# Performance work log

Hardware: AMD Instinct MI355X
Metric: run time of the kernel (lower is better)

Reference implementation:

```python
import jax, jax.numpy as jnp
import numpy as np

T, D, H = 2048, 2048, 16
C = D // H  # head dim = 128

def setup_inputs() -> dict:
    key = jax.random.key(0)
    k1, k2, k3 = jax.random.split(key, 3)
    x = jax.random.normal(k1, (T, D), dtype=jnp.float32)
    W_attn = jax.random.normal(k2, (3 * D, D), dtype=jnp.float32) * 0.02
    W_proj = jax.random.normal(k3, (D, D), dtype=jnp.float32) * 0.02
    return {"x": x, "W_attn": W_attn, "W_proj": W_proj}

def reference(x, W_attn, W_proj):
    # c_attn: per-token Linear -> [T, 3D]
    qkv = x @ W_attn.T
    q, k, v = jnp.split(qkv, 3, axis=-1)  # each [T, D]
    # [T, D] -> [H, T, C]
    q = q.reshape(T, H, C).transpose(1, 0, 2)
    k = k.reshape(T, H, C).transpose(1, 0, 2)
    v = v.reshape(T, H, C).transpose(1, 0, 2)
    # raw scores [H, T, T]
    scores = jnp.einsum('htc,hsc->hts', q, k)
    causal_mask = jnp.tril(jnp.ones((1, T, T))) == 0
    scores = jnp.where(causal_mask, float('-inf'), scores)
    orig_dtype = scores.dtype
    # NOTE: original scales AFTER masking, inside softmax, in fp32
    attn = jax.nn.softmax(scores.astype(jnp.float32) / jnp.sqrt(jnp.float32(C)), axis=-1)
    attn = attn.astype(orig_dtype)
    out = attn @ v  # [H, T, C]
    out = out.transpose(1, 0, 2).reshape(T, D)
    return out @ W_proj.T
```

## Files before the change

### kernel.cpp

```cpp
#include <hip/hip_runtime.h>
#include <hip/hip_bf16.h>
#include <stdint.h>

typedef __attribute__((ext_vector_type(8))) __bf16 bf16x8;
typedef __attribute__((ext_vector_type(4))) float f32x4;
typedef __attribute__((ext_vector_type(4))) unsigned int u32x4;
typedef __attribute__((ext_vector_type(4))) unsigned short u16x4;

__device__ __forceinline__ unsigned short f2bf(float f) {
  union { float f; unsigned int u; } v; v.f = f;
  unsigned int r = v.u + 0x7fffu + ((v.u >> 16) & 1u);
  return (unsigned short)(r >> 16);
}

__device__ __forceinline__ void gload_lds16(const void* g, void* l) {
  __builtin_amdgcn_global_load_lds(
      (const __attribute__((address_space(1))) unsigned int*)g,
      (__attribute__((address_space(3))) unsigned int*)l, 16, 0, 0);
}

__global__ __launch_bounds__(256) void cast_f32_bf16(const float* __restrict__ in,
                                                     unsigned short* __restrict__ out,
                                                     int n) {
  int i = (blockIdx.x * 256 + threadIdx.x) * 4;
  if (i >= n) return;
  f32x4 v = *(const f32x4*)&in[i];
  u16x4 o;
  o[0] = f2bf(v[0]); o[1] = f2bf(v[1]); o[2] = f2bf(v[2]); o[3] = f2bf(v[3]);
  *(u16x4*)&out[i] = o;
}

template<int OUT_BF16>
__global__ __launch_bounds__(256) void gemm_bt(const unsigned short* __restrict__ A,
                                               const unsigned short* __restrict__ B,
                                               void* __restrict__ Cv,
                                               int M, int N, int K) {
  __shared__ unsigned short As[128 * 32];
  __shared__ unsigned short Bs[128 * 32];

  const int tid  = threadIdx.x;
  const int lane = tid & 63;
  const int wave = tid >> 6;
  const int wr = (wave >> 1) * 64;
  const int wc = (wave & 1) * 64;
  const int row0 = blockIdx.y * 128;
  const int col0 = blockIdx.x * 128;
  const int l16 = lane & 15;
  const int lk  = (lane >> 4) * 8;

  const int srow = lane >> 2;
  const int sc   = (lane & 3) * 8;

  f32x4 acc[4][4] = {};

  for (int k0 = 0; k0 < K; k0 += 32) {
    __syncthreads();
#pragma unroll
    for (int i = 0; i < 2; ++i) {
      int t = wave * 2 + i;
      int r = t * 16 + srow;
      gload_lds16(&A[(size_t)(row0 + r) * K + k0 + sc], &As[t * 512]);
      gload_lds16(&B[(size_t)(col0 + r) * K + k0 + sc], &Bs[t * 512]);
    }
    __syncthreads();

    bf16x8 af[4], bfr[4];
#pragma unroll
    for (int i = 0; i < 4; ++i) af[i]  = *(const bf16x8*)&As[(wr + i * 16 + l16) * 32 + lk];
#pragma unroll
    for (int i = 0; i < 4; ++i) bfr[i] = *(const bf16x8*)&Bs[(wc + i * 16 + l16) * 32 + lk];
#pragma unroll
    for (int i = 0; i < 4; ++i)
#pragma unroll
      for (int j = 0; j < 4; ++j)
        acc[i][j] = __builtin_amdgcn_mfma_f32_16x16x32_bf16(af[i], bfr[j], acc[i][j], 0, 0, 0);
  }

  const int orow = (lane >> 4) * 4;
#pragma unroll
  for (int i = 0; i < 4; ++i)
#pragma unroll
    for (int j = 0; j < 4; ++j)
#pragma unroll
      for (int r = 0; r < 4; ++r) {
        size_t gr = row0 + wr + i * 16 + orow + r;
        size_t gc = col0 + wc + j * 16 + l16;
        float v = acc[i][j][r];
        if (OUT_BF16) ((unsigned short*)Cv)[gr * N + gc] = f2bf(v);
        else          ((float*)Cv)[gr * N + gc] = v;
      }
}

__global__ __launch_bounds__(256, 2) void attn_kernel(const unsigned short* __restrict__ qkv,
                                                      unsigned short* __restrict__ ctx) {
  __shared__ unsigned short Ks[64][136];
  __shared__ unsigned short VTs[128][72];
  __shared__ unsigned short Ps[4][16][72];

  const int tid  = threadIdx.x;
  const int lane = tid & 63;
  const int w    = tid >> 6;
  const int l16  = lane & 15;
  const int lk8  = (lane >> 4) * 8;

  const int flat = blockIdx.x + blockIdx.y * 32;
  int h, qb;
  if (flat < 256) { h = flat >> 5; qb = flat & 31; }
  else            { int f2 = flat - 256; h = 8 + (f2 >> 5); qb = 31 - (f2 & 31); }

  const int qrow = qb * 64 + w * 16;

  bf16x8 qf[4];
#pragma unroll
  for (int kk = 0; kk < 4; ++kk)
    qf[kk] = *(const bf16x8*)&qkv[(size_t)(qrow + l16) * 6144 + h * 128 + kk * 32 + lk8];

  f32x4 o[8] = {};
  float m[4], lsum[4];
#pragma unroll
  for (int r = 0; r < 4; ++r) { m[r] = -1e30f; lsum[r] = 0.f; }

  const float sscale = 0.08838834764831845f * 1.4426950408889634f;
  const int qg0 = qrow + (lane >> 4) * 4;

  const int t0v = (tid & 15) * 4;
  const int c0v = (tid >> 4) * 8;

  const int nkb = qb + 1;
  for (int kb = 0; kb < nkb; ++kb) {
    u32x4 kreg[4], vreg[4];
#pragma unroll
    for (int it = 0; it < 4; ++it) {
      int idx = it * 256 + tid;
      int row = idx >> 4, c0 = (idx & 15) * 8;
      kreg[it] = *(const u32x4*)&qkv[(size_t)(kb * 64 + row) * 6144 + 2048 + h * 128 + c0];
    }
#pragma unroll
    for (int r = 0; r < 4; ++r)
      vreg[r] = *(const u32x4*)&qkv[(size_t)(kb * 64 + t0v + r) * 6144 + 4096 + h * 128 + c0v];

    __syncthreads();

#pragma unroll
    for (int it = 0; it < 4; ++it) {
      int idx = it * 256 + tid;
      int row = idx >> 4, c0 = (idx & 15) * 8;
      *(u32x4*)&Ks[row][c0] = kreg[it];
    }
    {
      const unsigned short* p0 = (const unsigned short*)&vreg[0];
      const unsigned short* p1 = (const unsigned short*)&vreg[1];
      const unsigned short* p2 = (const unsigned short*)&vreg[2];
      const unsigned short* p3 = (const unsigned short*)&vreg[3];
#pragma unroll
      for (int j = 0; j < 8; ++j) {
        u16x4 wv; wv[0] = p0[j]; wv[1] = p1[j]; wv[2] = p2[j]; wv[3] = p3[j];
        *(u16x4*)&VTs[c0v + j][t0v] = wv;
      }
    }
    __syncthreads();

    f32x4 s[4] = {};
#pragma unroll
    for (int kk = 0; kk < 4; ++kk)
#pragma unroll
      for (int n = 0; n < 4; ++n) {
        bf16x8 kf = *(const bf16x8*)&Ks[n * 16 + l16][kk * 32 + lk8];
        s[n] = __builtin_amdgcn_mfma_f32_16x16x32_bf16(qf[kk], kf, s[n], 0, 0, 0);
      }

    const bool diag = (kb == qb);
    float rmax[4];
#pragma unroll
    for (int r = 0; r < 4; ++r) rmax[r] = -1e30f;
#pragma unroll
    for (int n = 0; n < 4; ++n) {
      int kg = kb * 64 + n * 16 + l16;
#pragma unroll
      for (int r = 0; r < 4; ++r) {
        float v = s[n][r] * sscale;
        if (diag && kg > qg0 + r) v = -1e30f;
        s[n][r] = v;
        rmax[r] = fmaxf(rmax[r], v);
      }
    }
#pragma unroll
    for (int d = 1; d < 16; d <<= 1)
#pragma unroll
      for (int r = 0; r < 4; ++r) rmax[r] = fmaxf(rmax[r], __shfl_xor(rmax[r], d));

    float alpha[4];
#pragma unroll
    for (int r = 0; r < 4; ++r) {
      float mn = fmaxf(m[r], rmax[r]);
      alpha[r] = exp2f(m[r] - mn);
      m[r] = mn;
    }
    float rsum[4] = {0.f, 0.f, 0.f, 0.f};
#pragma unroll
    for (int n = 0; n < 4; ++n)
#pragma unroll
      for (int r = 0; r < 4; ++r) {
        float p = exp2f(s[n][r] - m[r]);
        s[n][r] = p;
        rsum[r] += p;
      }
#pragma unroll
    for (int d = 1; d < 16; d <<= 1)
#pragma unroll
      for (int r = 0; r < 4; ++r) rsum[r] += __shfl_xor(rsum[r], d);
#pragma unroll
    for (int r = 0; r < 4; ++r) lsum[r] = lsum[r] * alpha[r] + rsum[r];

#pragma unroll
    for (int n = 0; n < 8; ++n)
#pragma unroll
      for (int r = 0; r < 4; ++r) o[n][r] *= alpha[r];

#pragma unroll
    for (int n = 0; n < 4; ++n)
#pragma unroll
      for (int r = 0; r < 4; ++r)
        Ps[w][(lane >> 4) * 4 + r][n * 16 + l16] = f2bf(s[n][r]);
    __syncthreads();

#pragma unroll
    for (int kk = 0; kk < 2; ++kk) {
      bf16x8 pf = *(const bf16x8*)&Ps[w][l16][kk * 32 + lk8];
#pragma unroll
      for (int n = 0; n < 8; ++n) {
        bf16x8 vf = *(const bf16x8*)&VTs[n * 16 + l16][kk * 32 + lk8];
        o[n] = __builtin_amdgcn_mfma_f32_16x16x32_bf16(pf, vf, o[n], 0, 0, 0);
      }
    }
  }

#pragma unroll
  for (int r = 0; r < 4; ++r) {
    float inv = 1.0f / lsum[r];
    size_t gr = qrow + (lane >> 4) * 4 + r;
#pragma unroll
    for (int n = 0; n < 8; ++n)
      ctx[gr * 2048 + h * 128 + n * 16 + l16] = f2bf(o[n][r] * inv);
  }
}

extern "C" void kernel_launch(void* const* d_in, const int* in_sizes, int n_in,
                              void* d_out, int out_size, void* d_ws, size_t ws_size,
                              hipStream_t stream) {
  const float* x  = (const float*)d_in[0];
  const float* Wa = (const float*)d_in[1];
  const float* Wp = (const float*)d_in[2];
  float* out = (float*)d_out;

  char* ws = (char*)d_ws;
  unsigned short* xb   = (unsigned short*)(ws);
  unsigned short* wab  = (unsigned short*)(ws + 8388608);
  unsigned short* wpb  = (unsigned short*)(ws + 33554432);
  unsigned short* qkvb = (unsigned short*)(ws + 41943040);
  unsigned short* ctx  = (unsigned short*)(ws + 67108864);

  cast_f32_bf16<<<4096, 256, 0, stream>>>(x, xb, 2048 * 2048);
  cast_f32_bf16<<<12288, 256, 0, stream>>>(Wa, wab, 6144 * 2048);
  cast_f32_bf16<<<4096, 256, 0, stream>>>(Wp, wpb, 2048 * 2048);

  gemm_bt<1><<<dim3(48, 16), 256, 0, stream>>>(xb, wab, qkvb, 2048, 6144, 2048);

  attn_kernel<<<dim3(32, 16), 256, 0, stream>>>(qkvb, ctx);

  gemm_bt<0><<<dim3(16, 16), 256, 0, stream>>>(ctx, wpb, out, 2048, 2048, 2048);
}
```

Baseline: 313.0 us.

## Double-buffer GEMM LDS tiles, XOR-swizzle attention LDS, drop per-wave barrier

The GEMM now uses two LDS buffers and issues the next K-tile's global-to-LDS loads before computing on the current tile, with a single barrier per iteration. This overlaps load latency with MFMA work. The attention kernel replaces padded shared arrays with XOR-swizzled indexing to avoid bank conflicts while using less LDS. The block-wide barrier after writing the per-wave P tile is replaced by an lgkmcnt wait, since only the owning wave reads it. The GEMM's direct-to-LDS loads are asynchronous (vmcnt), and no explicit vmcnt wait is added before the barrier, so correctness depends on the compiler inserting one.

```diff
diff --git a/kernel.cpp b/kernel.cpp
--- a/kernel.cpp
+++ b/kernel.cpp
@@ -35,8 +35,8 @@
                                                const unsigned short* __restrict__ B,
                                                void* __restrict__ Cv,
                                                int M, int N, int K) {
-  __shared__ unsigned short As[128 * 32];
-  __shared__ unsigned short Bs[128 * 32];
+  __shared__ unsigned short As[2][128 * 32];
+  __shared__ unsigned short Bs[2][128 * 32];
 
   const int tid  = threadIdx.x;
   const int lane = tid & 63;
@@ -53,27 +53,39 @@
 
   f32x4 acc[4][4] = {};
 
-  for (int k0 = 0; k0 < K; k0 += 32) {
-    __syncthreads();
-#pragma unroll
-    for (int i = 0; i < 2; ++i) {
-      int t = wave * 2 + i;
-      int r = t * 16 + srow;
-      gload_lds16(&A[(size_t)(row0 + r) * K + k0 + sc], &As[t * 512]);
-      gload_lds16(&B[(size_t)(col0 + r) * K + k0 + sc], &Bs[t * 512]);
-    }
-    __syncthreads();
+#pragma unroll
+  for (int i = 0; i < 2; ++i) {
+    int t = wave * 2 + i;
+    int r = t * 16 + srow;
+    gload_lds16(&A[(size_t)(row0 + r) * K + sc], &As[0][t * 512]);
+    gload_lds16(&B[(size_t)(col0 + r) * K + sc], &Bs[0][t * 512]);
+  }
+  __syncthreads();
+
+  int cur = 0;
+  for (int k0 = 0; k0 < K; k0 += 32, cur ^= 1) {
+    if (k0 + 32 < K) {
+#pragma unroll
+      for (int i = 0; i < 2; ++i) {
+        int t = wave * 2 + i;
+        int r = t * 16 + srow;
+        gload_lds16(&A[(size_t)(row0 + r) * K + k0 + 32 + sc], &As[cur ^ 1][t * 512]);
+        gload_lds16(&B[(size_t)(col0 + r) * K + k0 + 32 + sc], &Bs[cur ^ 1][t * 512]);
+      }
+    }
 
     bf16x8 af[4], bfr[4];
 #pragma unroll
-    for (int i = 0; i < 4; ++i) af[i]  = *(const bf16x8*)&As[(wr + i * 16 + l16) * 32 + lk];
-#pragma unroll
-    for (int i = 0; i < 4; ++i) bfr[i] = *(const bf16x8*)&Bs[(wc + i * 16 + l16) * 32 + lk];
+    for (int i = 0; i < 4; ++i) af[i]  = *(const bf16x8*)&As[cur][(wr + i * 16 + l16) * 32 + lk];
+#pragma unroll
+    for (int i = 0; i < 4; ++i) bfr[i] = *(const bf16x8*)&Bs[cur][(wc + i * 16 + l16) * 32 + lk];
 #pragma unroll
     for (int i = 0; i < 4; ++i)
 #pragma unroll
       for (int j = 0; j < 4; ++j)
         acc[i][j] = __builtin_amdgcn_mfma_f32_16x16x32_bf16(af[i], bfr[j], acc[i][j], 0, 0, 0);
+
+    __syncthreads();
   }
 
   const int orow = (lane >> 4) * 4;
@@ -91,11 +103,15 @@
       }
 }
 
+#define KS_IDX(r, c) ((((r) * 128) + (c)) ^ (((r) & 7) << 3))
+#define VT_IDX(c, t) ((((c) * 64)  + (t)) ^ (((c) & 7) << 3))
+#define PS_IDX(q, c) ((((q) * 64)  + (c)) ^ (((q) & 7) << 3))
+
 __global__ __launch_bounds__(256, 2) void attn_kernel(const unsigned short* __restrict__ qkv,
                                                       unsigned short* __restrict__ ctx) {
-  __shared__ unsigned short Ks[64][136];
-  __shared__ unsigned short VTs[128][72];
-  __shared__ unsigned short Ps[4][16][72];
+  __shared__ unsigned short Ks[64 * 128];
+  __shared__ unsigned short VTs[128 * 64];
+  __shared__ unsigned short Ps[4][16 * 64];
 
   const int tid  = threadIdx.x;
   const int lane = tid & 63;
@@ -145,7 +161,7 @@
     for (int it = 0; it < 4; ++it) {
       int idx = it * 256 + tid;
       int row = idx >> 4, c0 = (idx & 15) * 8;
-      *(u32x4*)&Ks[row][c0] = kreg[it];
+      *(u32x4*)&Ks[KS_IDX(row, c0)] = kreg[it];
     }
     {
       const unsigned short* p0 = (const unsigned short*)&vreg[0];
@@ -155,7 +171,7 @@
 #pragma unroll
       for (int j = 0; j < 8; ++j) {
         u16x4 wv; wv[0] = p0[j]; wv[1] = p1[j]; wv[2] = p2[j]; wv[3] = p3[j];
-        *(u16x4*)&VTs[c0v + j][t0v] = wv;
+        *(u16x4*)&VTs[VT_IDX(c0v + j, t0v)] = wv;
       }
     }
     __syncthreads();
@@ -165,7 +181,7 @@
     for (int kk = 0; kk < 4; ++kk)
 #pragma unroll
       for (int n = 0; n < 4; ++n) {
-        bf16x8 kf = *(const bf16x8*)&Ks[n * 16 + l16][kk * 32 + lk8];
+        bf16x8 kf = *(const bf16x8*)&Ks[KS_IDX(n * 16 + l16, kk * 32 + lk8)];
         s[n] = __builtin_amdgcn_mfma_f32_16x16x32_bf16(qf[kk], kf, s[n], 0, 0, 0);
       }
 
@@ -221,15 +237,15 @@
     for (int n = 0; n < 4; ++n)
 #pragma unroll
       for (int r = 0; r < 4; ++r)
-        Ps[w][(lane >> 4) * 4 + r][n * 16 + l16] = f2bf(s[n][r]);
-    __syncthreads();
+        Ps[w][PS_IDX((lane >> 4) * 4 + r, n * 16 + l16)] = f2bf(s[n][r]);
+    asm volatile("s_waitcnt lgkmcnt(0)" ::: "memory");
 
 #pragma unroll
     for (int kk = 0; kk < 2; ++kk) {
-      bf16x8 pf = *(const bf16x8*)&Ps[w][l16][kk * 32 + lk8];
+      bf16x8 pf = *(const bf16x8*)&Ps[w][PS_IDX(l16, kk * 32 + lk8)];
 #pragma unroll
       for (int n = 0; n < 8; ++n) {
-        bf16x8 vf = *(const bf16x8*)&VTs[n * 16 + l16][kk * 32 + lk8];
+        bf16x8 vf = *(const bf16x8*)&VTs[VT_IDX(n * 16 + l16, kk * 32 + lk8)];
         o[n] = __builtin_amdgcn_mfma_f32_16x16x32_bf16(pf, vf, o[n], 0, 0, 0);
       }
     }
```

New measurement: 301.0 us. 3.9% less time.
